# Performance work log

Hardware: AMD Instinct MI355X
Metric: run time of the kernel (lower is better)

Reference implementation:

```python
import jax, jax.numpy as jnp
import numpy as np

N = 100000       # n_nodes
E = 128          # hidden_channels
R = 9            # n_relations
L = 3            # n_layers
NE = 640000      # n_edges


def setup_inputs() -> dict:
    key = jax.random.key(0)
    k = jax.random.split(key, 5)
    edge_index = jax.random.randint(k[0], (2, NE), 0, N, dtype=jnp.int64)
    edge_type = jax.random.randint(k[1], (NE,), 0, R, dtype=jnp.int64)
    embeddings = jax.random.normal(k[2], (N, E), dtype=jnp.float32)
    # per-layer weights [L, 2R, E, E] (first R = forward direction, last R = reverse)
    weights = jax.random.normal(k[3], (L, 2 * R, E, E), dtype=jnp.float32)
    biases = jax.random.normal(k[4], (L, 2 * R, E), dtype=jnp.float32)
    return {
        "edge_index": edge_index,
        "edge_type": edge_type,
        "embeddings": embeddings,
        "weights": weights,
        "biases": biases,
    }


def reference(edge_index, edge_type, embeddings, weights, biases):
    src, dst = edge_index[0], edge_index[1]
    n_nodes = embeddings.shape[0]
    n_layers, r2 = weights.shape[0], weights.shape[1]
    n_rel = r2 // 2

    hidden = embeddings
    for l in range(n_layers):
        # NB: source code resets hidden to the embeddings at the top of each
        # layer, so each layer transforms the raw embeddings. We reproduce
        # that exactly (the relu in the source is dead code: its result is
        # immediately overwritten by `hidden = output`).
        hidden = embeddings
        # Transform node features once per relation (node-level GEMM) instead
        # of per-edge: mathematically identical to gathering then matmul.
        ht = jnp.einsum('ne,reh->rnh', hidden, weights[l])  # [2R, N, E]
        # forward direction: message = W_r @ h[src] + b_r, scattered to dst
        msg_f = ht[edge_type, src] + biases[l][edge_type]          # [NE, E]
        out = jax.ops.segment_sum(msg_f, dst, num_segments=n_nodes)
        # reverse direction: message = W_{r+R} @ h[dst] + b_{r+R}, scattered to src
        msg_b = ht[edge_type + n_rel, dst] + biases[l][edge_type + n_rel]
        out = out + jax.ops.segment_sum(msg_b, src, num_segments=n_nodes)
        hidden = out
    return hidden
```

## Files before the change

### kernel.cpp

```cpp
#include <hip/hip_runtime.h>
#include <hip/hip_bf16.h>


#define E_DIM 128
#define R_REL 9
#define TN 16
#define MT_P 1156
#define SCB 1024
#define NSLICE 96

typedef __attribute__((ext_vector_type(8))) short short8v;
typedef __attribute__((ext_vector_type(4))) float f32x4;

static __device__ __forceinline__ unsigned short f2bf(float f) {
    union { float f; unsigned u; } v; v.f = f;
    unsigned u = v.u;
    return (unsigned short)((u + 0x7FFFu + ((u >> 16) & 1u)) >> 16);
}
static __device__ __forceinline__ float bf2f(unsigned short h) {
    union { unsigned u; float f; } v; v.u = ((unsigned)h) << 16;
    return v.f;
}


__global__ __launch_bounds__(256) void prep(
    const float* __restrict__ H, const float* __restrict__ W18,
    unsigned short* __restrict__ Hbf, unsigned short* __restrict__ Wt,
    long total8)
{
    const int tid = threadIdx.x;
    if (blockIdx.x < 18) {
        const int rel = blockIdx.x;
        const float* __restrict__ Wr = W18 + (size_t)rel * E_DIM * E_DIM;
#pragma unroll
        for (int k = 0; k < 8; k++) {
            int f = tid + k * 256;
            int lane = f & 63;
            int c = (f >> 6) & 1;
            int s = (f >> 7) & 3;
            int w = (f >> 9) & 3;
            int col = w * 32 + c * 16 + (lane & 15);
            int kb = s * 32 + (lane >> 4) * 8;
            short8v v;
#pragma unroll
            for (int j = 0; j < 8; j++)
                v[j] = (short)f2bf(Wr[(size_t)(kb + j) * E_DIM + col]);
            *(short8v*)(Wt + ((size_t)((((rel * 4 + w) * 4 + s) * 2 + c) * 64 + lane)) * 8) = v;
        }
    } else {
        long i = (long)(blockIdx.x - 18) * 256 + tid;
        if (i >= total8) return;
        const float4* src = (const float4*)(H + i * 8);
        float4 a = src[0], b = src[1];
        short8v o;
        o[0] = (short)f2bf(a.x); o[1] = (short)f2bf(a.y);
        o[2] = (short)f2bf(a.z); o[3] = (short)f2bf(a.w);
        o[4] = (short)f2bf(b.x); o[5] = (short)f2bf(b.y);
        o[6] = (short)f2bf(b.z); o[7] = (short)f2bf(b.w);
        *(short8v*)(Hbf + i * 8) = o;
    }
}

__global__ __launch_bounds__(256) void k_count8(
    const int* __restrict__ esrc, const int* __restrict__ edst,
    const int* __restrict__ etype, int* __restrict__ cnt, int ne, int Nn)
{
    const int oct = blockIdx.x & 7;
    const int slice = blockIdx.x >> 3;
    const int lo = (int)(((long long)oct * Nn) >> 3);
    const int hi = (int)(((long long)(oct + 1) * Nn) >> 3);
    for (int e = slice * 256 + threadIdx.x; e < ne; e += NSLICE * 256) {
        int t = etype[e], s = esrc[e], d = edst[e];
        if (d >= lo && d < hi) atomicAdd(&cnt[d * R_REL + t], 1);
        if (s >= lo && s < hi) atomicAdd(&cnt[(Nn + s) * R_REL + t], 1);
    }
}

__global__ __launch_bounds__(256) void k_scan_part(
    const int* __restrict__ cnt, int* __restrict__ loc,
    int* __restrict__ bsum, int n2)
{
    __shared__ int sh[256];
    const int tid = threadIdx.x;
    const int i0 = blockIdx.x * SCB + tid * 4;
    int v0 = 0, v1 = 0, v2 = 0, v3 = 0;
    if (i0 + 3 < n2) {
        int4 v = *(const int4*)(cnt + i0);
        v0 = v.x; v1 = v.y; v2 = v.z; v3 = v.w;
    } else {
        if (i0 + 0 < n2) v0 = cnt[i0 + 0];
        if (i0 + 1 < n2) v1 = cnt[i0 + 1];
        if (i0 + 2 < n2) v2 = cnt[i0 + 2];
        if (i0 + 3 < n2) v3 = cnt[i0 + 3];
    }
    int t = v0 + v1 + v2 + v3;
    sh[tid] = t;
    __syncthreads();
    for (int o = 1; o < 256; o <<= 1) {
        int x = (tid >= o) ? sh[tid - o] : 0;
        __syncthreads();
        sh[tid] += x;
        __syncthreads();
    }
    int excl = sh[tid] - t;
    if (tid == 255) bsum[blockIdx.x] = sh[255];
    int p0 = excl, p1 = p0 + v0, p2 = p1 + v1, p3 = p2 + v2;
    if (i0 + 3 < n2) {
        *(int4*)(loc + i0) = make_int4(p0, p1, p2, p3);
    } else {
        if (i0 + 0 < n2) loc[i0 + 0] = p0;
        if (i0 + 1 < n2) loc[i0 + 1] = p1;
        if (i0 + 2 < n2) loc[i0 + 2] = p2;
        if (i0 + 3 < n2) loc[i0 + 3] = p3;
    }
}

__global__ __launch_bounds__(256) void k_scan_mid(int* __restrict__ bsum, int nb)
{
    __shared__ int sh[256];
    __shared__ int carry;
    const int tid = threadIdx.x;
    if (tid == 0) carry = 0;
    __syncthreads();
    for (int base = 0; base < nb; base += 256) {
        int i = base + tid;
        int v = (i < nb) ? bsum[i] : 0;
        sh[tid] = v;
        __syncthreads();
        for (int o = 1; o < 256; o <<= 1) {
            int x = (tid >= o) ? sh[tid - o] : 0;
            __syncthreads();
            sh[tid] += x;
            __syncthreads();
        }
        int excl = sh[tid] - v + carry;
        int total = sh[255];
        if (i < nb) bsum[i] = excl;
        __syncthreads();
        if (tid == 0) carry += total;
        __syncthreads();
    }
}

__global__ __launch_bounds__(256) void k_scan_apply(
    const int* __restrict__ loc, const int* __restrict__ bsum,
    int* __restrict__ off, int* __restrict__ cursor, int n2)
{
    const int add = bsum[blockIdx.x];
    const int i0 = blockIdx.x * SCB + threadIdx.x * 4;
    if (i0 + 3 < n2) {
        int4 v = *(const int4*)(loc + i0);
        v.x += add; v.y += add; v.z += add; v.w += add;
        *(int4*)(off + i0) = v;
        *(int4*)(cursor + i0) = v;
    } else {
#pragma unroll
        for (int j = 0; j < 4; j++)
            if (i0 + j < n2) {
                int v = loc[i0 + j] + add;
                off[i0 + j] = v;
                cursor[i0 + j] = v;
            }
    }
}

__global__ __launch_bounds__(256) void k_fill8(
    const int* __restrict__ esrc, const int* __restrict__ edst,
    const int* __restrict__ etype, int* __restrict__ cursor,
    unsigned* __restrict__ rec, int ne, int Nn)
{
    const int oct = blockIdx.x & 7;
    const int slice = blockIdx.x >> 3;
    const int lo = (int)(((long long)oct * Nn) >> 3);
    const int hi = (int)(((long long)(oct + 1) * Nn) >> 3);
    for (int e = slice * 256 + threadIdx.x; e < ne; e += NSLICE * 256) {
        int t = etype[e], s = esrc[e], d = edst[e];
        if (d >= lo && d < hi) {
            int p = atomicAdd(&cursor[d * R_REL + t], 1);
            rec[p] = ((unsigned)t << 20) | (unsigned)s;
        }
        if (s >= lo && s < hi) {
            int p2 = atomicAdd(&cursor[(Nn + s) * R_REL + t], 1);
            rec[p2] = ((unsigned)t << 20) | (unsigned)d;
        }
    }
}

__global__ __launch_bounds__(256, 4) void fused_rgcn(
    const unsigned short* __restrict__ Hbf, const unsigned short* __restrict__ Wt,
    const float* __restrict__ B18,
    const int* __restrict__ off3, const int* __restrict__ cur3,
    const unsigned* __restrict__ rec,
    float* __restrict__ out, int Nn)
{
    __shared__ __align__(16) unsigned short Mt[TN][MT_P];
    __shared__ float degS[2][TN][R_REL];

    const int tid = threadIdx.x;
    const int lane = tid & 63;
    const int w = tid >> 6;
    const int lr = lane & 15;
    const int lg = lane >> 4;
    const int grp = lg;
    const int gl = lr;
    const int n0 = blockIdx.x * TN;

    const short8v* wt8 = (const short8v*)Wt;
    const short8v z8 = (short8v){0, 0, 0, 0, 0, 0, 0, 0};

    f32x4 acc[2];
    acc[0] = (f32x4){0.f, 0.f, 0.f, 0.f};
    acc[1] = (f32x4){0.f, 0.f, 0.f, 0.f};

#define RMW(rk, vk)                                                           \
    {                                                                         \
        int _t = (int)((rk) >> 20);                                           \
        unsigned short* _mp = &Mt[w * 4 + grp][_t * E_DIM + gl * 8];          \
        short8v _m = *(short8v*)_mp;                                          \
        _Pragma("unroll")                                                     \
        for (int _c = 0; _c < 8; _c++) {                                      \
            float _f = bf2f((unsigned short)_m[_c]) +                         \
                       bf2f((unsigned short)(vk)[_c]);                        \
            _m[_c] = (short)f2bf(_f);                                         \
        }                                                                     \
        *(short8v*)_mp = _m;                                                  \
    }

#pragma unroll 1
    for (int dir = 0; dir < 2; dir++) {
#pragma unroll
        for (int rr = 0; rr < 4; rr++) {
            int row = w * 4 + rr;
            *(short8v*)(&Mt[row][(size_t)lane * 8]) = z8;
            *(short8v*)(&Mt[row][(size_t)(lane + 64) * 8]) = z8;
            if (lane < 16) *(short8v*)(&Mt[row][(size_t)(lane + 128) * 8]) = z8;
        }

        const int jj = lg, tt = lr;
        const int gnode_j = n0 + w * 4 + jj;
        int blo = 0x7F000000, bhi = 0x7F000000;
        if (gnode_j < Nn && tt < R_REL) {
            size_t sb = ((size_t)(dir ? (Nn + gnode_j) : gnode_j)) * R_REL + tt;
            blo = off3[sb];
            bhi = cur3[sb];
            degS[dir][w * 4 + jj][tt] = (float)(bhi - blo);
        }

        const int st_g = __shfl(blo, grp * 16 + 0);
        const int en_g = __shfl(bhi, grp * 16 + 8);

        int ii = st_g;
        while (__any(ii < en_g)) {
            bool a0 = ii + 0 < en_g;
            bool a1 = ii + 1 < en_g;
            bool a2 = ii + 2 < en_g;
            bool a3 = ii + 3 < en_g;
            unsigned r0 = 0, r1 = 0, r2 = 0, r3 = 0;
            if (a0) r0 = rec[ii + 0];
            if (a1) r1 = rec[ii + 1];
            if (a2) r2 = rec[ii + 2];
            if (a3) r3 = rec[ii + 3];
            short8v v0 = z8, v1 = z8, v2 = z8, v3 = z8;
            if (a0) v0 = *(const short8v*)(Hbf + (size_t)(r0 & 0xFFFFF) * E_DIM + gl * 8);
            if (a1) v1 = *(const short8v*)(Hbf + (size_t)(r1 & 0xFFFFF) * E_DIM + gl * 8);
            if (a2) v2 = *(const short8v*)(Hbf + (size_t)(r2 & 0xFFFFF) * E_DIM + gl * 8);
            if (a3) v3 = *(const short8v*)(Hbf + (size_t)(r3 & 0xFFFFF) * E_DIM + gl * 8);
            if (a0) RMW(r0, v0);
            if (a1) RMW(r1, v1);
            if (a2) RMW(r2, v2);
            if (a3) RMW(r3, v3);
            ii += 4;
        }
        __syncthreads();

#pragma unroll 1
        for (int q = 0; q < R_REL; q++) {
            const int rel = dir * R_REL + q;
#pragma unroll
            for (int s = 0; s < 4; s++) {
                short8v b0 = wt8[(size_t)((((rel * 4 + w) * 4 + s) * 2 + 0) * 64) + lane];
                short8v b1 = wt8[(size_t)((((rel * 4 + w) * 4 + s) * 2 + 1) * 64) + lane];
                short8v a = *(const short8v*)(&Mt[lr][q * E_DIM + s * 32 + lg * 8]);
                acc[0] = __builtin_amdgcn_mfma_f32_16x16x32_bf16(b0, a, acc[0], 0, 0, 0);
                acc[1] = __builtin_amdgcn_mfma_f32_16x16x32_bf16(b1, a, acc[1], 0, 0, 0);
            }
        }
        __syncthreads();
    }
#undef RMW

    const int gnode = n0 + lr;
    if (gnode >= Nn) return;
#pragma unroll 1
    for (int dir = 0; dir < 2; dir++) {
#pragma unroll 1
        for (int t = 0; t < R_REL; t++) {
            float dg = degS[dir][lr][t];
            if (dg != 0.f) {
                const float* brow = B18 + (size_t)(dir * R_REL + t) * E_DIM + w * 32 + lg * 4;
                float4 b0 = *(const float4*)(brow);
                float4 b1 = *(const float4*)(brow + 16);
                acc[0][0] += dg * b0.x; acc[0][1] += dg * b0.y;
                acc[0][2] += dg * b0.z; acc[0][3] += dg * b0.w;
                acc[1][0] += dg * b1.x; acc[1][1] += dg * b1.y;
                acc[1][2] += dg * b1.z; acc[1][3] += dg * b1.w;
            }
        }
    }
    float* po = out + (size_t)gnode * E_DIM + w * 32 + lg * 4;
    *(float4*)po = make_float4(acc[0][0], acc[0][1], acc[0][2], acc[0][3]);
    *(float4*)(po + 16) = make_float4(acc[1][0], acc[1][1], acc[1][2], acc[1][3]);
}


__global__ __launch_bounds__(128) void direct_edge(
    const int* __restrict__ esrc, const int* __restrict__ edst,
    const int* __restrict__ etype,
    const float* __restrict__ H, const float* __restrict__ W2,
    const float* __restrict__ B2, float* __restrict__ out, int ne)
{
    __shared__ float hs[E_DIM];
    __shared__ float hd[E_DIM];
    int e = blockIdx.x;
    if (e >= ne) return;
    int t = etype[e], s = esrc[e], d = edst[e];
    int c = threadIdx.x;
    hs[c] = H[(size_t)s * E_DIM + c];
    hd[c] = H[(size_t)d * E_DIM + c];
    __syncthreads();
    const float* Wf = W2 + (size_t)t * E_DIM * E_DIM;
    const float* Wb = W2 + (size_t)(t + R_REL) * E_DIM * E_DIM;
    float accf = B2[(size_t)t * E_DIM + c];
    float accb = B2[(size_t)(t + R_REL) * E_DIM + c];
#pragma unroll 8
    for (int k = 0; k < E_DIM; k++) {
        accf += hs[k] * Wf[(size_t)k * E_DIM + c];
        accb += hd[k] * Wb[(size_t)k * E_DIM + c];
    }
    atomicAdd(&out[(size_t)d * E_DIM + c], accf);
    atomicAdd(&out[(size_t)s * E_DIM + c], accb);
}

extern "C" void kernel_launch(void* const* d_in, const int* in_sizes, int n_in,
                              void* d_out, int out_size, void* d_ws, size_t ws_size,
                              hipStream_t stream) {
    const int* edge_index = (const int*)d_in[0];
    const int* edge_type  = (const int*)d_in[1];
    const float* emb      = (const float*)d_in[2];
    const float* weights  = (const float*)d_in[3];
    const float* biases   = (const float*)d_in[4];
    float* out = (float*)d_out;

    const int NE = in_sizes[1];
    const int Nn = in_sizes[2] / E_DIM;
    const int L  = in_sizes[3] / (2 * R_REL * E_DIM * E_DIM);

    const float* W2 = weights + (size_t)(L - 1) * 2 * R_REL * E_DIM * E_DIM;
    const float* B2 = biases  + (size_t)(L - 1) * 2 * R_REL * E_DIM;

    const int* esrc = edge_index;
    const int* edst = edge_index + NE;

    const int n3 = 2 * Nn * R_REL;
    const int nb3 = (n3 + SCB - 1) / SCB;

    auto al = [](size_t x) { return (x + 255) & ~(size_t)255; };
    const size_t hbfBytes = al((size_t)Nn * E_DIM * 2);
    const size_t wtBytes  = al((size_t)2 * R_REL * E_DIM * E_DIM * 2);
    const size_t offBytes = al((size_t)n3 * 4);
    const size_t curBytes = al((size_t)n3 * 4);
    const size_t recBytes = al((size_t)2 * NE * 4);
    const size_t bsBytes  = al((size_t)nb3 * 4);
    const size_t need = hbfBytes + wtBytes + offBytes + curBytes + recBytes + bsBytes;

    if (ws_size >= need && Nn < (1 << 20)) {
        char* p = (char*)d_ws;
        unsigned short* Hbf = (unsigned short*)p;        p += hbfBytes;
        unsigned short* Wt  = (unsigned short*)p;        p += wtBytes;
        int* off3           = (int*)p;                   p += offBytes;
        int* cur3           = (int*)p;                   p += curBytes;
        unsigned* rec       = (unsigned*)p;              p += recBytes;
        int* bsum           = (int*)p;

        const long total8 = (long)Nn * (E_DIM / 8);
        const int hblocks = (int)((total8 + 255) / 256);

        hipMemsetAsync(off3, 0, (size_t)n3 * 4, stream);
        prep<<<18 + hblocks, 256, 0, stream>>>(emb, W2, Hbf, Wt, total8);
        k_count8<<<8 * NSLICE, 256, 0, stream>>>(esrc, edst, edge_type, off3, NE, Nn);
        k_scan_part<<<nb3, 256, 0, stream>>>(off3, cur3, bsum, n3);
        k_scan_mid<<<1, 256, 0, stream>>>(bsum, nb3);
        k_scan_apply<<<nb3, 256, 0, stream>>>(cur3, bsum, off3, cur3, n3);
        k_fill8<<<8 * NSLICE, 256, 0, stream>>>(esrc, edst, edge_type,
                                                cur3, rec, NE, Nn);

        fused_rgcn<<<(Nn + TN - 1) / TN, 256, 0, stream>>>(
            Hbf, Wt, B2, off3, cur3, rec, out, Nn);
        return;
    }

    hipMemsetAsync(d_out, 0, (size_t)Nn * E_DIM * sizeof(float), stream);
    direct_edge<<<NE, 128, 0, stream>>>(esrc, edst, edge_type, emb, W2, B2, out, NE);
}
```

Baseline: 414.6 us.

## Chunk relation aggregation into groups of three to shrink LDS and raise occupancy

The per-block shared-memory aggregation buffer held all 9 relations per node (16x1156 bf16). It now holds 3 relations (16x392), and the gather/accumulate and MFMA phases loop over three relation chunks per direction. This cuts LDS use by about 3x, and launch bounds rise from 4 to 8 blocks per SM so more waves can hide gather latency. In exchange there are more __syncthreads and zeroing passes, and register pressure is tighter under the higher occupancy target.

```diff
diff --git a/kernel.cpp b/kernel.cpp
--- a/kernel.cpp
+++ b/kernel.cpp
@@ -5,7 +5,8 @@
 #define E_DIM 128
 #define R_REL 9
 #define TN 16
-#define MT_P 1156
+#define TCH 3
+#define MT_P2 392
 #define SCB 1024
 #define NSLICE 96
 
@@ -186,14 +187,14 @@
     }
 }
 
-__global__ __launch_bounds__(256, 4) void fused_rgcn(
+__global__ __launch_bounds__(256, 8) void fused_rgcn(
     const unsigned short* __restrict__ Hbf, const unsigned short* __restrict__ Wt,
     const float* __restrict__ B18,
     const int* __restrict__ off3, const int* __restrict__ cur3,
     const unsigned* __restrict__ rec,
     float* __restrict__ out, int Nn)
 {
-    __shared__ __align__(16) unsigned short Mt[TN][MT_P];
+    __shared__ __align__(16) unsigned short Mt[TN][MT_P2];
     __shared__ float degS[2][TN][R_REL];
 
     const int tid = threadIdx.x;
@@ -212,30 +213,22 @@
     acc[0] = (f32x4){0.f, 0.f, 0.f, 0.f};
     acc[1] = (f32x4){0.f, 0.f, 0.f, 0.f};
 
-#define RMW(rk, vk)                                                           \
+#define RMW(rk, vk, tbase)                                                    \
     {                                                                         \
-        int _t = (int)((rk) >> 20);                                           \
-        unsigned short* _mp = &Mt[w * 4 + grp][_t * E_DIM + gl * 8];          \
+        int _tl = (int)((rk) >> 20) - (tbase);                                \
+        unsigned short* _mp = &Mt[w * 4 + grp][_tl * E_DIM + gl * 8];         \
         short8v _m = *(short8v*)_mp;                                          \
         _Pragma("unroll")                                                     \
         for (int _c = 0; _c < 8; _c++) {                                      \
             float _f = bf2f((unsigned short)_m[_c]) +                         \
                        bf2f((unsigned short)(vk)[_c]);                        \
-            _m[_c] = (short)f2bf(_f);                                         \
+            _m[_c] = (short)f2bf(_f);                                        \
         }                                                                     \
         *(short8v*)_mp = _m;                                                  \
     }
 
 #pragma unroll 1
     for (int dir = 0; dir < 2; dir++) {
-#pragma unroll
-        for (int rr = 0; rr < 4; rr++) {
-            int row = w * 4 + rr;
-            *(short8v*)(&Mt[row][(size_t)lane * 8]) = z8;
-            *(short8v*)(&Mt[row][(size_t)(lane + 64) * 8]) = z8;
-            if (lane < 16) *(short8v*)(&Mt[row][(size_t)(lane + 128) * 8]) = z8;
-        }
-
         const int jj = lg, tt = lr;
         const int gnode_j = n0 + w * 4 + jj;
         int blo = 0x7F000000, bhi = 0x7F000000;
@@ -246,46 +239,56 @@
             degS[dir][w * 4 + jj][tt] = (float)(bhi - blo);
         }
 
-        const int st_g = __shfl(blo, grp * 16 + 0);
-        const int en_g = __shfl(bhi, grp * 16 + 8);
-
-        int ii = st_g;
-        while (__any(ii < en_g)) {
-            bool a0 = ii + 0 < en_g;
-            bool a1 = ii + 1 < en_g;
-            bool a2 = ii + 2 < en_g;
-            bool a3 = ii + 3 < en_g;
-            unsigned r0 = 0, r1 = 0, r2 = 0, r3 = 0;
-            if (a0) r0 = rec[ii + 0];
-            if (a1) r1 = rec[ii + 1];
-            if (a2) r2 = rec[ii + 2];
-            if (a3) r3 = rec[ii + 3];
-            short8v v0 = z8, v1 = z8, v2 = z8, v3 = z8;
-            if (a0) v0 = *(const short8v*)(Hbf + (size_t)(r0 & 0xFFFFF) * E_DIM + gl * 8);
-            if (a1) v1 = *(const short8v*)(Hbf + (size_t)(r1 & 0xFFFFF) * E_DIM + gl * 8);
-            if (a2) v2 = *(const short8v*)(Hbf + (size_t)(r2 & 0xFFFFF) * E_DIM + gl * 8);
-            if (a3) v3 = *(const short8v*)(Hbf + (size_t)(r3 & 0xFFFFF) * E_DIM + gl * 8);
-            if (a0) RMW(r0, v0);
-            if (a1) RMW(r1, v1);
-            if (a2) RMW(r2, v2);
-            if (a3) RMW(r3, v3);
-            ii += 4;
-        }
-        __syncthreads();
-
 #pragma unroll 1
-        for (int q = 0; q < R_REL; q++) {
-            const int rel = dir * R_REL + q;
-#pragma unroll
-            for (int s = 0; s < 4; s++) {
-                short8v b0 = wt8[(size_t)((((rel * 4 + w) * 4 + s) * 2 + 0) * 64) + lane];
-                short8v b1 = wt8[(size_t)((((rel * 4 + w) * 4 + s) * 2 + 1) * 64) + lane];
-                short8v a = *(const short8v*)(&Mt[lr][q * E_DIM + s * 32 + lg * 8]);
-                acc[0] = __builtin_amdgcn_mfma_f32_16x16x32_bf16(b0, a, acc[0], 0, 0, 0);
-                acc[1] = __builtin_amdgcn_mfma_f32_16x16x32_bf16(b1, a, acc[1], 0, 0, 0);
+        for (int ch = 0; ch < 3; ch++) {
+            const int tbase = ch * TCH;
+#pragma unroll
+            for (int rr = 0; rr < 4; rr++) {
+                if (lane < 48)
+                    *(short8v*)(&Mt[w * 4 + rr][(size_t)lane * 8]) = z8;
             }
-        }
-        __syncthreads();
+
+            const int st_g = __shfl(blo, grp * 16 + tbase);
+            const int en_g = __shfl(bhi, grp * 16 + tbase + TCH - 1);
+
+            int ii = st_g;
+            while (__any(ii < en_g)) {
+                bool a0 = ii + 0 < en_g;
+                bool a1 = ii + 1 < en_g;
+                bool a2 = ii + 2 < en_g;
+                bool a3 = ii + 3 < en_g;
+                unsigned r0 = 0, r1 = 0, r2 = 0, r3 = 0;
+                if (a0) r0 = rec[ii + 0];
+                if (a1) r1 = rec[ii + 1];
+                if (a2) r2 = rec[ii + 2];
+                if (a3) r3 = rec[ii + 3];
+                short8v v0 = z8, v1 = z8, v2 = z8, v3 = z8;
+                if (a0) v0 = *(const short8v*)(Hbf + (size_t)(r0 & 0xFFFFF) * E_DIM + gl * 8);
+                if (a1) v1 = *(const short8v*)(Hbf + (size_t)(r1 & 0xFFFFF) * E_DIM + gl * 8);
+                if (a2) v2 = *(const short8v*)(Hbf + (size_t)(r2 & 0xFFFFF) * E_DIM + gl * 8);
+                if (a3) v3 = *(const short8v*)(Hbf + (size_t)(r3 & 0xFFFFF) * E_DIM + gl * 8);
+                if (a0) RMW(r0, v0, tbase);
+                if (a1) RMW(r1, v1, tbase);
+                if (a2) RMW(r2, v2, tbase);
+                if (a3) RMW(r3, v3, tbase);
+                ii += 4;
+            }
+            __syncthreads();
+
+#pragma unroll
+            for (int q = 0; q < TCH; q++) {
+                const int rel = dir * R_REL + tbase + q;
+#pragma unroll
+                for (int s = 0; s < 4; s++) {
+                    short8v b0 = wt8[(size_t)((((rel * 4 + w) * 4 + s) * 2 + 0) * 64) + lane];
+                    short8v b1 = wt8[(size_t)((((rel * 4 + w) * 4 + s) * 2 + 1) * 64) + lane];
+                    short8v a = *(const short8v*)(&Mt[lr][q * E_DIM + s * 32 + lg * 8]);
+                    acc[0] = __builtin_amdgcn_mfma_f32_16x16x32_bf16(b0, a, acc[0], 0, 0, 0);
+                    acc[1] = __builtin_amdgcn_mfma_f32_16x16x32_bf16(b1, a, acc[1], 0, 0, 0);
+                }
+            }
+            __syncthreads();
+        }
     }
 #undef RMW
 
```

Result: faster. 348.5 us (-16.0%).
